# Performance work log

Hardware: AMD Instinct MI355X
Metric: run time of the kernel (lower is better)

## Reference

```python
import jax, jax.numpy as jnp
import numpy as np

BS, T, X_DIM = 16, 4096, 256


def setup_inputs() -> dict:
    key = jax.random.key(0)
    kx, kb, kl = jax.random.split(key, 3)
    x_set = jax.random.normal(kx, (BS, T, X_DIM), dtype=jnp.float32)
    # Match torch.nn.init.orthogonal_ via QR of a Gaussian matrix
    B, _ = jnp.linalg.qr(jax.random.normal(kb, (X_DIM, X_DIM), dtype=jnp.float32))
    Lam, _ = jnp.linalg.qr(jax.random.normal(kl, (X_DIM, X_DIM), dtype=jnp.float32))
    return {"x_set": x_set, "B": B.astype(jnp.float32), "Lam": Lam.astype(jnp.float32)}


def reference(x_set, B, Lam):
    # Original computes h_T = sum_{j=0}^{T} Lambda^j @ B @ x_{T-j} (O(T^2)).
    # Equivalent linear recurrence: h_t = Lambda @ h_{t-1} + B @ x_t, h_{-1} = 0.
    Bx = jnp.einsum('de,bte->btd', B, x_set)          # [bs, T, d]

    def step(h, bx_t):
        h = jnp.einsum('de,be->bd', Lam, h) + bx_t    # [bs, d]
        return h, h

    h0 = jnp.zeros((x_set.shape[0], x_set.shape[2]), dtype=x_set.dtype)
    _, hs = jax.lax.scan(step, h0, jnp.swapaxes(Bx, 0, 1))  # [T, bs, d]
    return jnp.swapaxes(hs, 0, 1)                            # [bs, T, d]
```

## Files before the change

kernel.cpp:

```cpp
#include <hip/hip_runtime.h>
#include <hip/hip_bf16.h>
#include <stdint.h>


#define CHUNK  64

typedef short v8s __attribute__((ext_vector_type(8)));
typedef float v4f __attribute__((ext_vector_type(4)));

static __device__ __forceinline__ unsigned short f2u(float f) {
  union { float f; unsigned int u; } x; x.f = f;
  unsigned int u = x.u + 0x7FFFu + ((x.u >> 16) & 1u);
  return (unsigned short)(u >> 16);
}
static __device__ __forceinline__ float u2f(unsigned short h) {
  union { unsigned int u; float f; } x; x.u = ((unsigned int)h) << 16;
  return x.f;
}
static __device__ __forceinline__ void lds_barrier() {
  asm volatile("s_waitcnt lgkmcnt(0)\n\ts_barrier" ::: "memory");
}

template<bool A_F32, bool C_BF16, bool ADD_C>
__global__ __launch_bounds__(256) void gemm_tile(
    const void* __restrict__ Ap, const unsigned short* __restrict__ Bp,
    void* __restrict__ Cp, int lda, int ldb, int ldc, int Kper, long csplit)
{
  __shared__ unsigned short As[64][72];
  __shared__ unsigned short Bst[64][72];
  const int tid = threadIdx.x;
  const int lane = tid & 63, w = tid >> 6;
  const int q = lane >> 4, ln = lane & 15;
  const long n0 = (long)blockIdx.x * 64;
  const long m0 = (long)blockIdx.y * 64;
  const int  kz = blockIdx.z;
  const long kbase = (long)kz * Kper;
  const int sm = tid >> 2;
  const int sk = (tid & 3) << 4;

  v4f acc[4];
#pragma unroll
  for (int i = 0; i < 4; ++i) acc[i] = 0;

  float4 fA[4];
  v8s aR0, aR1, bR0, bR1;

  auto load_tile = [&](long kg) {
    if (A_F32) {
      const float* A = (const float*)Ap + (m0 + sm) * (long)lda + kg + sk;
#pragma unroll
      for (int t = 0; t < 4; ++t) fA[t] = ((const float4*)A)[t];
    } else {
      const unsigned short* A = (const unsigned short*)Ap + (m0 + sm) * (long)lda + kg + sk;
      aR0 = ((const v8s*)A)[0]; aR1 = ((const v8s*)A)[1];
    }
    const unsigned short* Bg = Bp + (kg + sm) * (long)ldb + n0 + sk;
    bR0 = ((const v8s*)Bg)[0]; bR1 = ((const v8s*)Bg)[1];
  };

  load_tile(kbase);

  for (int ks = 0; ks < Kper; ks += 64) {
    __syncthreads();
    if (A_F32) {
      unsigned short* d = &As[sm][sk];
#pragma unroll
      for (int t = 0; t < 4; ++t) {
        d[4*t+0] = f2u(fA[t].x); d[4*t+1] = f2u(fA[t].y);
        d[4*t+2] = f2u(fA[t].z); d[4*t+3] = f2u(fA[t].w);
      }
    } else {
      *(v8s*)&As[sm][sk] = aR0; *(v8s*)&As[sm][sk + 8] = aR1;
    }
#pragma unroll
    for (int r = 0; r < 8; ++r) Bst[sk + r][sm] = (unsigned short)bR0[r];
#pragma unroll
    for (int r = 0; r < 8; ++r) Bst[sk + 8 + r][sm] = (unsigned short)bR1[r];
    __syncthreads();
    if (ks + 64 < Kper) load_tile(kbase + ks + 64);
#pragma unroll
    for (int kb = 0; kb < 64; kb += 32) {
      v8s a = *(const v8s*)&As[w*16 + ln][kb + q*8];
#pragma unroll
      for (int nb = 0; nb < 4; ++nb) {
        v8s b = *(const v8s*)&Bst[nb*16 + ln][kb + q*8];
        acc[nb] = __builtin_amdgcn_mfma_f32_16x16x32_bf16(a, b, acc[nb], 0, 0, 0);
      }
    }
  }
#pragma unroll
  for (int nb = 0; nb < 4; ++nb)
#pragma unroll
    for (int r = 0; r < 4; ++r) {
      const long row = m0 + w*16 + q*4 + r;
      const long col = n0 + nb*16 + ln;
      float v = acc[nb][r];
      if (C_BF16) ((unsigned short*)Cp)[row * (long)ldc + col] = f2u(v);
      else {
        float* Cf = (float*)Cp + (long)kz * csplit;
        if (ADD_C) v += Cf[row * (long)ldc + col];
        Cf[row * (long)ldc + col] = v;
      }
    }
}

__global__ __launch_bounds__(512) void pow_round(
    unsigned short* __restrict__ Phi, unsigned short* __restrict__ Plo, int mpow,
    unsigned short* __restrict__ Phi2, unsigned short* __restrict__ Plo2)
{
  __shared__ unsigned short As[64][136];
  __shared__ unsigned short Bst[64][136];
  const int tid = threadIdx.x, lane = tid & 63, w = tid >> 6;
  const int q = lane >> 4, ln = lane & 15;
  const int jj = (blockIdx.x >> 2) + 1;
  const int n0 = (blockIdx.x & 3) * 64;
  const int m0 = blockIdx.y * 64;
  const int mb = w >> 1, nh = w & 1;
  const unsigned short* Ah = Phi + (size_t)mpow * 65536;
  const unsigned short* Al = Plo + (size_t)mpow * 65536;
  const unsigned short* Bh = Phi + (size_t)jj * 65536;
  const unsigned short* Bl = Plo + (size_t)jj * 65536;
  const int sm  = tid >> 3, sk  = (tid & 7) << 4;
  const int smk = tid >> 2, snk = (tid & 3) << 4;
  v4f acc[2];
#pragma unroll
  for (int i = 0; i < 2; ++i) acc[i] = 0;

  v8s aR0, aR1, bR0, bR1;
  auto load_tile = [&](int it) {
    const int seg = it >> 1, ks = (it & 1) << 7;
    const unsigned short* Asrc = (seg == 1) ? Al : Ah;
    const unsigned short* Bsrc = (seg == 2) ? Bl : Bh;
    const unsigned short* Ag = Asrc + (size_t)(m0 + sm) * 256 + ks + sk;
    aR0 = ((const v8s*)Ag)[0]; aR1 = ((const v8s*)Ag)[1];
    const unsigned short* Bg = Bsrc + (size_t)(ks + smk) * 256 + n0 + snk;
    bR0 = ((const v8s*)Bg)[0]; bR1 = ((const v8s*)Bg)[1];
  };

  load_tile(0);
  for (int it = 0; it < 6; ++it) {
    __syncthreads();
    *(v8s*)&As[sm][sk] = aR0; *(v8s*)&As[sm][sk + 8] = aR1;
#pragma unroll
    for (int r = 0; r < 8; ++r) Bst[snk + r][smk] = (unsigned short)bR0[r];
#pragma unroll
    for (int r = 0; r < 8; ++r) Bst[snk + 8 + r][smk] = (unsigned short)bR1[r];
    __syncthreads();
    if (it + 1 < 6) load_tile(it + 1);
#pragma unroll
    for (int kb = 0; kb < 128; kb += 32) {
      v8s a = *(const v8s*)&As[mb*16 + ln][kb + q*8];
#pragma unroll
      for (int nb = 0; nb < 2; ++nb) {
        v8s bb = *(const v8s*)&Bst[nh*32 + nb*16 + ln][kb + q*8];
        acc[nb] = __builtin_amdgcn_mfma_f32_16x16x32_bf16(a, bb, acc[nb], 0, 0, 0);
      }
    }
  }
  const size_t ob = (size_t)(mpow + jj) * 65536;
#pragma unroll
  for (int nb = 0; nb < 2; ++nb)
#pragma unroll
    for (int r = 0; r < 4; ++r) {
      const int row = m0 + mb*16 + q*4 + r;
      const int col = n0 + nh*32 + nb*16 + ln;
      float v = acc[nb][r];
      unsigned short hi = f2u(v);
      Phi[ob + (size_t)row*256 + col] = hi;
      Plo[ob + (size_t)row*256 + col] = f2u(v - u2f(hi));
      if (mpow == 32) {
        if (jj == 32) {
          Phi2[65536 + (size_t)row*256 + col] = hi;
          Plo2[65536 + (size_t)row*256 + col] = f2u(v - u2f(hi));
        } else if (jj == 1) {
          Phi2[(size_t)row*256 + col] = (row == col) ? (unsigned short)0x3F80 : (unsigned short)0;
          Plo2[(size_t)row*256 + col] = 0;
        }
      }
    }
}

__global__ __launch_bounds__(256) void pack_init(
    const float* __restrict__ Bm, const float* __restrict__ Lam,
    unsigned short* __restrict__ Bt, unsigned short* __restrict__ LamT,
    unsigned short* __restrict__ Phi, unsigned short* __restrict__ Plo)
{
  const int idx = blockIdx.x * 256 + threadIdx.x;
  const int e = idx >> 8, d = idx & 255;
  Bt[idx]   = f2u(Bm[d * 256 + e]);
  LamT[idx] = f2u(Lam[d * 256 + e]);
  float v = Lam[idx];
  unsigned short hi = f2u(v);
  Phi[65536 + idx] = hi;
  Plo[65536 + idx] = f2u(v - u2f(hi));
  const int dd = idx >> 8, ee = idx & 255;
  Phi[idx] = (dd == ee) ? (unsigned short)0x3F80 : (unsigned short)0;
  Plo[idx] = 0;
}

__global__ __launch_bounds__(256) void pack_all(
    const unsigned short* __restrict__ Phi,
    const unsigned short* __restrict__ Phi2, const unsigned short* __restrict__ Plo2,
    unsigned short* __restrict__ Ghat,
    unsigned short* __restrict__ Qcat, unsigned short* __restrict__ G2,
    unsigned short* __restrict__ LcT2hi, unsigned short* __restrict__ LcT2lo)
{
  __shared__ unsigned short tile[64][65];
  const int tx = threadIdx.x & 63, ty = threadIdx.x >> 6;
  const int blk0 = blockIdx.x;
  if (blk0 < 1024) {
    const int jpar = blk0 >> 4, t16 = blk0 & 15;
    const unsigned short* src = Phi + (size_t)(63 - jpar) * 65536;
    const int d0 = (t16 & 3) * 64, e0 = (t16 >> 2) * 64;
#pragma unroll
    for (int s = 0; s < 16; ++s)
      tile[ty*16 + s][tx] = src[(size_t)(d0 + ty*16 + s) * 256 + e0 + tx];
    __syncthreads();
#pragma unroll
    for (int s = 0; s < 16; ++s) {
      const int e = e0 + ty*16 + s, d = d0 + tx;
      Ghat[((size_t)(jpar*256 + e)) * 256 + d] = tile[tx][ty*16 + s];
    }
    return;
  }
  const int blk = blk0 - 1024;
  if (blk < 1152) {
    const int rt = blk >> 5, ct = blk & 31;
    const int k0 = rt * 64, c0 = ct * 64;
    const int r = c0 >> 8, d0 = c0 & 255;
    int p = 0, e0 = 0;
    bool zero = false;
    if (k0 < 256) { p = r; e0 = k0; }
    else {
      const int u = (k0 - 256) >> 8; e0 = (k0 - 256) & 255;
      if (u >= r) zero = true; else p = r - 1 - u;
    }
    if (zero) {
#pragma unroll
      for (int s = 0; s < 16; ++s)
        Qcat[(size_t)(k0 + ty*16 + s) * 2048 + c0 + tx] = 0;
      return;
    }
    const unsigned short* src = Phi2 + (size_t)p * 65536;
#pragma unroll
    for (int s = 0; s < 16; ++s)
      tile[ty*16 + s][tx] = src[(size_t)(d0 + ty*16 + s) * 256 + e0 + tx];
    __syncthreads();
#pragma unroll
    for (int s = 0; s < 16; ++s)
      Qcat[(size_t)(k0 + ty*16 + s) * 2048 + c0 + tx] = tile[tx][ty*16 + s];
  } else if (blk < 1280) {
    const int t = blk - 1152;
    const int rt = t >> 2, ct = t & 3;
    const int k0 = rt * 64, d0 = ct * 64;
    const int r = k0 >> 8, e0 = k0 & 255;
    const unsigned short* src = Phi2 + (size_t)(7 - r) * 65536;
#pragma unroll
    for (int s = 0; s < 16; ++s)
      tile[ty*16 + s][tx] = src[(size_t)(d0 + ty*16 + s) * 256 + e0 + tx];
    __syncthreads();
#pragma unroll
    for (int s = 0; s < 16; ++s)
      G2[(size_t)(k0 + ty*16 + s) * 256 + d0 + tx] = tile[tx][ty*16 + s];
  } else {
    const int t = blk - 1280;
    const int half = t >> 4, t16 = t & 15;
    const int d0 = (t16 & 3) * 64, e0 = (t16 >> 2) * 64;
    const unsigned short* src = (half ? Plo2 : Phi2) + (size_t)8 * 65536;
    unsigned short* dst = half ? LcT2lo : LcT2hi;
#pragma unroll
    for (int s = 0; s < 16; ++s)
      tile[ty*16 + s][tx] = src[(size_t)(d0 + ty*16 + s) * 256 + e0 + tx];
    __syncthreads();
#pragma unroll
    for (int s = 0; s < 16; ++s)
      dst[(size_t)(e0 + ty*16 + s) * 256 + d0 + tx] = tile[tx][ty*16 + s];
  }
}

__global__ __launch_bounds__(256) void reduce_s2(
    const float* __restrict__ Sp, unsigned short* __restrict__ Acat)
{
  const int f = blockIdx.x * 256 + threadIdx.x;
  float v = 0;
#pragma unroll
  for (int z = 0; z < 8; ++z) v += Sp[(size_t)z * 262144 + f];
  const int e = f & 255, i = (f >> 8) & 63, b = f >> 14;
  const int u = i & 7, m = i >> 3;
  Acat[(size_t)(b*8 + m) * 2304 + 256 + u*256 + e] = f2u(v);
}

__global__ __launch_bounds__(512, 2) void k4b_combine(
    const unsigned short* __restrict__ LcT2hi, const unsigned short* __restrict__ LcT2lo,
    const float* __restrict__ S2, unsigned short* __restrict__ Acat)
{
  __shared__ unsigned short Hhi[16][264];
  __shared__ unsigned short Hlo[16][264];
  const int tid = threadIdx.x, lane = tid & 63, w = tid >> 6;
  const int q = lane >> 4, ln = lane & 15;

  v8s bhi[8][2], blo[8][2];
#pragma unroll
  for (int kk = 0; kk < 8; ++kk)
#pragma unroll
    for (int nb = 0; nb < 2; ++nb) {
      const int n = 32*w + nb*16 + ln;
#pragma unroll
      for (int r = 0; r < 8; ++r) {
        const int k = kk*32 + q*8 + r;
        bhi[kk][nb][r] = (short)LcT2hi[k*256 + n];
        blo[kk][nb][r] = (short)LcT2lo[k*256 + n];
      }
    }
  for (int e = tid; e < 16*264; e += 512) { (&Hhi[0][0])[e] = 0; (&Hlo[0][0])[e] = 0; }
  lds_barrier();

  for (int m = 0; m < 8; ++m) {
    for (int e = tid; e < 4096; e += 512) {
      const int b = e >> 8, d = e & 255;
      Acat[(size_t)(b*8 + m) * 2304 + d] = Hhi[b][d];
    }
    v8s ahi[8], alo[8];
#pragma unroll
    for (int kk = 0; kk < 8; ++kk) {
      ahi[kk] = *(const v8s*)&Hhi[ln][kk*32 + q*8];
      alo[kk] = *(const v8s*)&Hlo[ln][kk*32 + q*8];
    }
    lds_barrier();
    v4f acc[2];
#pragma unroll
    for (int nb = 0; nb < 2; ++nb)
#pragma unroll
      for (int r = 0; r < 4; ++r) {
        const int bb = 4*q + r, col = 32*w + nb*16 + ln;
        acc[nb][r] = S2[(size_t)(bb*8 + m) * 256 + col];
      }
#pragma unroll
    for (int kk = 0; kk < 8; ++kk)
#pragma unroll
      for (int nb = 0; nb < 2; ++nb) {
        acc[nb] = __builtin_amdgcn_mfma_f32_16x16x32_bf16(ahi[kk], bhi[kk][nb], acc[nb], 0, 0, 0);
        acc[nb] = __builtin_amdgcn_mfma_f32_16x16x32_bf16(alo[kk], bhi[kk][nb], acc[nb], 0, 0, 0);
        acc[nb] = __builtin_amdgcn_mfma_f32_16x16x32_bf16(ahi[kk], blo[kk][nb], acc[nb], 0, 0, 0);
      }
#pragma unroll
    for (int nb = 0; nb < 2; ++nb)
#pragma unroll
      for (int r = 0; r < 4; ++r) {
        const int bb = 4*q + r, col = 32*w + nb*16 + ln;
        float v = acc[nb][r];
        unsigned short hi = f2u(v);
        Hhi[bb][col] = hi;
        Hlo[bb][col] = f2u(v - u2f(hi));
      }
    lds_barrier();
  }
}

__global__ __launch_bounds__(256, 1) void k5_scan(
    const unsigned short* __restrict__ LamT,
    const unsigned short* __restrict__ Bx,
    const unsigned short* __restrict__ Abf, float* __restrict__ Out)
{
  __shared__ unsigned short gs[2][16][264];
  const int tid = threadIdx.x, lane = tid & 63, w = tid >> 6;
  const int q = lane >> 4, ln = lane & 15;
  const int blk = blockIdx.x;
  const int b  = blk >> 4;
  const int i0 = (blk * 4) & 63;

  v8s bf[8][4];
#pragma unroll
  for (int kk = 0; kk < 8; ++kk)
#pragma unroll
    for (int nb = 0; nb < 4; ++nb) {
      const int n = 64*w + nb*16 + ln;
#pragma unroll
      for (int r = 0; r < 8; ++r)
        bf[kk][nb][r] = (short)LamT[(kk*32 + q*8 + r) * 256 + n];
    }
  for (int e = tid; e < 2*16*264; e += 256) (&gs[0][0][0])[e] = 0;
  lds_barrier();
#pragma unroll
  for (int r = 0; r < 4; ++r)
    gs[0][4*r][tid] = Abf[((size_t)(b*64 + i0 + r)) * 256 + tid];

  const size_t baseq = ((size_t)b*4096 + (size_t)(i0 + q)*64) * 256;
  const int colw = 64*w;

  unsigned short bxr[2][4];
#pragma unroll
  for (int s = 0; s < 2; ++s)
#pragma unroll
    for (int nb = 0; nb < 4; ++nb)
      bxr[s][nb] = Bx[baseq + (size_t)s*256 + colw + nb*16 + ln];
  lds_barrier();

#pragma unroll 2
  for (int j = 0; j < CHUNK; ++j) {
    v8s a[8];
#pragma unroll
    for (int kk = 0; kk < 8; ++kk) a[kk] = *(const v8s*)&gs[j & 1][ln][kk*32 + q*8];
    v4f acc[4];
#pragma unroll
    for (int nb = 0; nb < 4; ++nb) acc[nb] = 0;
#pragma unroll
    for (int kk = 0; kk < 8; ++kk)
#pragma unroll
      for (int nb = 0; nb < 4; ++nb)
        acc[nb] = __builtin_amdgcn_mfma_f32_16x16x32_bf16(a[kk], bf[kk][nb], acc[nb], 0, 0, 0);
    {
      const size_t rb = baseq + (size_t)j*256 + colw;
#pragma unroll
      for (int nb = 0; nb < 4; ++nb) {
        const float g = acc[nb][0] + u2f(bxr[j & 1][nb]);
        Out[rb + nb*16 + ln] = g;
        gs[(j + 1) & 1][4*q][colw + nb*16 + ln] = f2u(g);
      }
      if (j < CHUNK - 2) {
        const size_t rb2 = baseq + (size_t)(j + 2)*256 + colw;
#pragma unroll
        for (int nb = 0; nb < 4; ++nb)
          bxr[j & 1][nb] = Bx[rb2 + nb*16 + ln];
      }
    }
    lds_barrier();
  }
}

extern "C" void kernel_launch(void* const* d_in, const int* in_sizes, int n_in,
                              void* d_out, int out_size, void* d_ws, size_t ws_size,
                              hipStream_t stream)
{
  const float* x   = (const float*)d_in[0];
  const float* Bm  = (const float*)d_in[1];
  const float* Lam = (const float*)d_in[2];
  float* Out = (float*)d_out;
  (void)in_sizes; (void)n_in; (void)out_size; (void)ws_size;

  char* ws = (char*)d_ws;
  size_t off = 0;
  auto alloc = [&](size_t bytes) { void* p = ws + off; off += (bytes + 255) & ~(size_t)255; return p; };
  unsigned short* Bx    = (unsigned short*)alloc((size_t)16777216 * 2);
  unsigned short* Phi   = (unsigned short*)alloc((size_t)65 * 65536 * 2);
  unsigned short* Plo   = (unsigned short*)alloc((size_t)65 * 65536 * 2);
  unsigned short* Ghat  = (unsigned short*)alloc((size_t)16384 * 256 * 2);
  unsigned short* Qcat  = (unsigned short*)alloc((size_t)2304 * 2048 * 2);
  unsigned short* G2    = (unsigned short*)alloc((size_t)2048 * 256 * 2);
  unsigned short* Phi2  = (unsigned short*)alloc((size_t)9 * 65536 * 2);
  unsigned short* Plo2  = (unsigned short*)alloc((size_t)9 * 65536 * 2);
  unsigned short* Bt    = (unsigned short*)alloc(131072);
  unsigned short* LamT  = (unsigned short*)alloc(131072);
  unsigned short* LcT2hi= (unsigned short*)alloc(131072);
  unsigned short* LcT2lo= (unsigned short*)alloc(131072);
  unsigned short* Acat  = (unsigned short*)alloc((size_t)128 * 2304 * 2);
  float*          S2    = (float*)alloc(131072);
  unsigned short* Abf   = (unsigned short*)alloc(524288);
  float*          Spart = (float*)Plo;

  pack_init<<<dim3(256), dim3(256), 0, stream>>>(Bm, Lam, Bt, LamT, Phi, Plo);
  gemm_tile<true, true, false><<<dim3(4, 1024, 1), dim3(256), 0, stream>>>(
      (const void*)x, Bt, (void*)Bx, 256, 256, 256, 256, 0);
  for (int mp = 1; mp <= 32; mp <<= 1)
    pow_round<<<dim3(mp * 4, 4, 1), dim3(512), 0, stream>>>(Phi, Plo, mp, Phi2, Plo2);
  for (int mp = 1; mp <= 4; mp <<= 1)
    pow_round<<<dim3(mp * 4, 4, 1), dim3(512), 0, stream>>>(Phi2, Plo2, mp, Phi2, Plo2);
  pack_all<<<dim3(2336), dim3(256), 0, stream>>>(Phi, Phi2, Plo2,
      Ghat, Qcat, G2, LcT2hi, LcT2lo);
  gemm_tile<false, false, false><<<dim3(4, 16, 8), dim3(256), 0, stream>>>(
      (const void*)Bx, Ghat, (void*)Spart, 16384, 256, 256, 2048, 262144);
  reduce_s2<<<dim3(1024), dim3(256), 0, stream>>>(Spart, Acat);
  gemm_tile<false, false, false><<<dim3(4, 2, 1), dim3(256), 0, stream>>>(
      (const void*)(Acat + 256), G2, (void*)S2, 2304, 256, 256, 2048, 0);
  k4b_combine<<<dim3(1), dim3(512), 0, stream>>>(LcT2hi, LcT2lo, S2, Acat);
  gemm_tile<false, true, false><<<dim3(32, 2, 1), dim3(256), 0, stream>>>(
      (const void*)Acat, Qcat, (void*)Abf, 2304, 2048, 2048, 2304, 0);
  k5_scan<<<dim3(256), dim3(256), 0, stream>>>(LamT, Bx, Abf, Out);
}
```

Before: 366.9 us.

## Add wide-N GEMM kernel covering full 256 columns per block

Adds a gemm_wide kernel in which each block computes a 64x256 output tile, so the A operand (including the fp32-to-bf16 conversion of x) is loaded and converted once rather than four times across column blocks. It is used for the Bx projection GEMM and the split-K Spart GEMM. In exchange, each block needs a larger LDS footprint, 16 accumulator vectors per thread, and a B transpose done with scalar LDS stores. The Spart GEMM launches far fewer blocks (128), which may underfill the GPU.

```diff
diff --git a/kernel.cpp b/kernel.cpp
--- a/kernel.cpp
+++ b/kernel.cpp
@@ -19,6 +19,88 @@
 }
 static __device__ __forceinline__ void lds_barrier() {
   asm volatile("s_waitcnt lgkmcnt(0)\n\ts_barrier" ::: "memory");
+}
+
+template<bool A_F32, bool C_BF16>
+__global__ __launch_bounds__(256) void gemm_wide(
+    const void* __restrict__ Ap, const unsigned short* __restrict__ Bp,
+    void* __restrict__ Cp, int lda, int ldb, int ldc, int Kper, long csplit)
+{
+  __shared__ unsigned short As[64][72];
+  __shared__ unsigned short Bst[256][72];
+  const int tid = threadIdx.x;
+  const int lane = tid & 63, w = tid >> 6;
+  const int q = lane >> 4, ln = lane & 15;
+  const long m0 = (long)blockIdx.x * 64;
+  const int  kz = blockIdx.y;
+  const long kbase = (long)kz * Kper;
+  const int sm = tid >> 2;
+  const int sk = (tid & 3) << 4;
+  const int bk = tid >> 2;
+  const int bn = (tid & 3) << 6;
+
+  v4f acc[16];
+#pragma unroll
+  for (int i = 0; i < 16; ++i) acc[i] = 0;
+
+  float4 fA[4];
+  v8s aR0, aR1, bR[8];
+
+  auto load_tile = [&](long kg) {
+    if (A_F32) {
+      const float* A = (const float*)Ap + (m0 + sm) * (long)lda + kg + sk;
+#pragma unroll
+      for (int t = 0; t < 4; ++t) fA[t] = ((const float4*)A)[t];
+    } else {
+      const unsigned short* A = (const unsigned short*)Ap + (m0 + sm) * (long)lda + kg + sk;
+      aR0 = ((const v8s*)A)[0]; aR1 = ((const v8s*)A)[1];
+    }
+    const unsigned short* Bg = Bp + (kg + bk) * (long)ldb + bn;
+#pragma unroll
+    for (int t = 0; t < 8; ++t) bR[t] = ((const v8s*)Bg)[t];
+  };
+
+  load_tile(kbase);
+
+  for (int ks = 0; ks < Kper; ks += 64) {
+    __syncthreads();
+    if (A_F32) {
+      unsigned short* d = &As[sm][sk];
+#pragma unroll
+      for (int t = 0; t < 4; ++t) {
+        d[4*t+0] = f2u(fA[t].x); d[4*t+1] = f2u(fA[t].y);
+        d[4*t+2] = f2u(fA[t].z); d[4*t+3] = f2u(fA[t].w);
+      }
+    } else {
+      *(v8s*)&As[sm][sk] = aR0; *(v8s*)&As[sm][sk + 8] = aR1;
+    }
+#pragma unroll
+    for (int c = 0; c < 8; ++c)
+#pragma unroll
+      for (int r = 0; r < 8; ++r)
+        Bst[bn + c*8 + r][bk] = (unsigned short)bR[c][r];
+    __syncthreads();
+    if (ks + 64 < Kper) load_tile(kbase + ks + 64);
+#pragma unroll
+    for (int kb = 0; kb < 64; kb += 32) {
+      v8s a = *(const v8s*)&As[w*16 + ln][kb + q*8];
+#pragma unroll
+      for (int nb = 0; nb < 16; ++nb) {
+        v8s b = *(const v8s*)&Bst[nb*16 + ln][kb + q*8];
+        acc[nb] = __builtin_amdgcn_mfma_f32_16x16x32_bf16(a, b, acc[nb], 0, 0, 0);
+      }
+    }
+  }
+#pragma unroll
+  for (int nb = 0; nb < 16; ++nb)
+#pragma unroll
+    for (int r = 0; r < 4; ++r) {
+      const long row = m0 + w*16 + q*4 + r;
+      const long col = nb*16 + ln;
+      float v = acc[nb][r];
+      if (C_BF16) ((unsigned short*)Cp)[row * (long)ldc + col] = f2u(v);
+      else ((float*)Cp + (long)kz * csplit)[row * (long)ldc + col] = v;
+    }
 }
 
 template<bool A_F32, bool C_BF16, bool ADD_C>
@@ -459,7 +541,7 @@
   float*          Spart = (float*)Plo;
 
   pack_init<<<dim3(256), dim3(256), 0, stream>>>(Bm, Lam, Bt, LamT, Phi, Plo);
-  gemm_tile<true, true, false><<<dim3(4, 1024, 1), dim3(256), 0, stream>>>(
+  gemm_wide<true, true><<<dim3(1024, 1), dim3(256), 0, stream>>>(
       (const void*)x, Bt, (void*)Bx, 256, 256, 256, 256, 0);
   for (int mp = 1; mp <= 32; mp <<= 1)
     pow_round<<<dim3(mp * 4, 4, 1), dim3(512), 0, stream>>>(Phi, Plo, mp, Phi2, Plo2);
@@ -467,7 +549,7 @@
     pow_round<<<dim3(mp * 4, 4, 1), dim3(512), 0, stream>>>(Phi2, Plo2, mp, Phi2, Plo2);
   pack_all<<<dim3(2336), dim3(256), 0, stream>>>(Phi, Phi2, Plo2,
       Ghat, Qcat, G2, LcT2hi, LcT2lo);
-  gemm_tile<false, false, false><<<dim3(4, 16, 8), dim3(256), 0, stream>>>(
+  gemm_wide<false, false><<<dim3(16, 8), dim3(256), 0, stream>>>(
       (const void*)Bx, Ghat, (void*)Spart, 16384, 256, 256, 2048, 262144);
   reduce_s2<<<dim3(1024), dim3(256), 0, stream>>>(Spart, Acat);
   gemm_tile<false, false, false><<<dim3(4, 2, 1), dim3(256), 0, stream>>>(
```

After: 408.8 us. 11.4% more time.
